# Optimization experiments

Hardware: AMD Instinct MI355X
Metric: run time of the kernel (lower is better)

Reference implementation:

```python
import jax, jax.numpy as jnp
import numpy as np


def setup_inputs() -> dict:
    key = jax.random.key(0)
    k1, k2, k3, k4, k5 = jax.random.split(key, 5)
    B, T, R, H = 64, 256, 49, 1024  # batch, caption len, regions (7x7), hidden
    V = jax.random.normal(k1, (B, R, H), dtype=jnp.float32)
    h_t = jax.random.normal(k2, (B, T, H), dtype=jnp.float32)
    Wv = jax.random.normal(k3, (R, H), dtype=jnp.float32) * (1.0 / np.sqrt(H))
    Wg = jax.random.normal(k4, (R, H), dtype=jnp.float32) * (1.0 / np.sqrt(H))
    Wh = jax.random.normal(k5, (1, R), dtype=jnp.float32) * (1.0 / np.sqrt(R))
    return {"V": V, "h_t": h_t, "Wv": Wv, "Wg": Wg, "Wh": Wh}


def reference(V, h_t, Wv, Wg, Wh):
    # content_v: [B,1,R,R] + [B,T,1,R] -> [B,T,R,R]
    cv = jnp.einsum('brh,kh->brk', V, Wv)      # [B, R, R]
    cg = jnp.einsum('bth,kh->btk', h_t, Wg)    # [B, T, R]
    content_v = cv[:, None, :, :] + cg[:, :, None, :]  # [B, T, R, R]
    # z_t = affine_h(tanh(content_v)) squeezed -> [B, T, R]
    z_t = jnp.einsum('btrk,k->btr', jnp.tanh(content_v), Wh[0])
    alpha_t = jax.nn.softmax(z_t, axis=-1)     # [B, T, R]
    c_t = jnp.einsum('btr,brh->bth', alpha_t, V)  # [B, T, H]
    return (c_t, alpha_t)
```

## Files before the change

### kernel.cpp

```cpp
#include <hip/hip_runtime.h>
#include <hip/hip_bf16.h>
#include <math.h>
#include <stdint.h>


typedef __attribute__((ext_vector_type(8))) short bf16x8;
typedef __attribute__((ext_vector_type(4))) float floatx4;

static __device__ __forceinline__ bf16x8 pack8(float4 a, float4 b) {
    union { __hip_bfloat162 h[4]; bf16x8 v; } u;
    u.h[0] = __float22bfloat162_rn(make_float2(a.x, a.y));
    u.h[1] = __float22bfloat162_rn(make_float2(a.z, a.w));
    u.h[2] = __float22bfloat162_rn(make_float2(b.x, b.y));
    u.h[3] = __float22bfloat162_rn(make_float2(b.z, b.w));
    return u.v;
}

static __device__ __forceinline__ unsigned short f2bf_bits(float f) {
    union { __hip_bfloat16 h; unsigned short u; } c;
    c.h = __float2bfloat16(f);
    return c.u;
}

__global__ __launch_bounds__(256) void gemm_mfma_tr(const float* __restrict__ Av,
                                                    const float* __restrict__ Ag,
                                                    const float* __restrict__ Wv,
                                                    const float* __restrict__ Wg,
                                                    float* __restrict__ Cv,
                                                    float* __restrict__ Cg,
                                                    unsigned short* __restrict__ vT) {
    __shared__ __align__(16) char smem[49 * 132 * 4];
    const int bid = blockIdx.x;
    const int tid = threadIdx.x;

    if (bid >= 610) {
        float* Ts = (float*)smem;
        const int tb = bid - 610;
        const int b = tb >> 3;
        const int h0 = (tb & 7) * 128;
        for (int i = tid; i < 49 * 32; i += 256) {
            const int r = i >> 5, hq = i & 31;
            *(float4*)(Ts + r * 132 + hq * 4) =
                *(const float4*)(Av + ((size_t)b * 49 + r) * 1024 + h0 + hq * 4);
        }
        __syncthreads();
        const int h = tid & 127;
        const int half = tid >> 7;
        float f[32];
#pragma unroll
        for (int j = 0; j < 32; ++j) {
            const int r = half * 32 + j;
            f[j] = (r < 49) ? Ts[r * 132 + h] : 0.f;
        }
        const size_t rowbase = ((size_t)b * 1024 + h0 + h) * 64;
#pragma unroll
        for (int o2 = 0; o2 < 4; ++o2) {
            const int o = half * 4 + o2;
            bf16x8 v = pack8(make_float4(f[o2*8+0], f[o2*8+1], f[o2*8+2], f[o2*8+3]),
                             make_float4(f[o2*8+4], f[o2*8+5], f[o2*8+6], f[o2*8+7]));
            *(bf16x8*)(vT + rowbase + (size_t)((o ^ (h & 7)) * 8)) = v;
        }
        return;
    }

    short* As = (short*)smem;
    short* Ws = (short*)(smem + 4096);
    const float* A; const float* W; float* C; int m0;
    if (bid < 98) { A = Av; W = Wv; C = Cv; m0 = bid * 32; }
    else          { A = Ag; W = Wg; C = Cg; m0 = (bid - 98) * 32; }

    const int wave = tid >> 6, lane = tid & 63;
    const int quad = lane >> 4, l16 = lane & 15;
    const int mb = (wave & 1) * 16;
    const int nb = (wave >> 1) * 32;

    floatx4 acc[2] = {};

    const int arow = tid >> 3, ag = tid & 7;
    const int wrow = tid >> 2, wq = tid & 3;
    const float* aptr = A + (size_t)(m0 + arow) * 1024 + ag * 8;
    const bool wvalid = wrow < 49;
    const float* wptr = W + (size_t)wrow * 1024 + wq * 16;

    float4 a0 = *(const float4*)(aptr);
    float4 a1 = *(const float4*)(aptr + 4);
    float4 w0 = make_float4(0.f,0.f,0.f,0.f), w1 = w0, w2 = w0, w3 = w0;
    if (wvalid) {
        w0 = *(const float4*)(wptr);
        w1 = *(const float4*)(wptr + 4);
        w2 = *(const float4*)(wptr + 8);
        w3 = *(const float4*)(wptr + 12);
    }

    for (int kc = 0; kc < 1024; kc += 64) {
        __syncthreads();
        *(bf16x8*)(As + arow * 64 + (ag ^ (arow & 7)) * 8) = pack8(a0, a1);
        *(bf16x8*)(Ws + wrow * 64 + ((wq * 2) ^ (wrow & 7)) * 8) = pack8(w0, w1);
        *(bf16x8*)(Ws + wrow * 64 + ((wq * 2 + 1) ^ (wrow & 7)) * 8) = pack8(w2, w3);
        __syncthreads();
        if (kc < 960) {
            a0 = *(const float4*)(aptr + kc + 64);
            a1 = *(const float4*)(aptr + kc + 68);
            if (wvalid) {
                w0 = *(const float4*)(wptr + kc + 64);
                w1 = *(const float4*)(wptr + kc + 68);
                w2 = *(const float4*)(wptr + kc + 72);
                w3 = *(const float4*)(wptr + kc + 76);
            }
        }
#pragma unroll
        for (int s = 0; s < 2; ++s) {
            const int am = mb + l16;
            bf16x8 af = *(const bf16x8*)(As + am * 64 + (((s << 2) + quad) ^ (am & 7)) * 8);
#pragma unroll
            for (int nt = 0; nt < 2; ++nt) {
                const int wn = nb + nt * 16 + l16;
                bf16x8 bf = *(const bf16x8*)(Ws + wn * 64 + (((s << 2) + quad) ^ (wn & 7)) * 8);
                acc[nt] = __builtin_amdgcn_mfma_f32_16x16x32_bf16(af, bf, acc[nt], 0, 0, 0);
            }
        }
    }

#pragma unroll
    for (int nt = 0; nt < 2; ++nt) {
        const int n = nb + nt * 16 + l16;
        if (n < 49) {
#pragma unroll
            for (int r = 0; r < 4; ++r) {
                const int m = m0 + mb + quad * 4 + r;
                C[(size_t)m * 49 + n] = acc[nt][r];
            }
        }
    }
}

__global__ __launch_bounds__(256) void zsoftmax(const float* __restrict__ cv,
                                                const float* __restrict__ cg,
                                                const float* __restrict__ Wh,
                                                float* __restrict__ alpha,
                                                unsigned short* __restrict__ a16) {
    const int b = blockIdx.x >> 4;
    const int t0 = (blockIdx.x & 15) * 16;
    __shared__ __align__(16) float cvl[49 * 52];
    __shared__ __align__(16) float cgl[16 * 52];
    __shared__ __align__(16) float whl[52];

    const int tid = threadIdx.x;
    for (int i = tid; i < 49 * 49; i += 256) {
        int r = i / 49, k = i - r * 49;
        cvl[r * 52 + k] = cv[(size_t)b * 2401 + i];
    }
    for (int i = tid; i < 16 * 49; i += 256) {
        int t = i / 49, k = i - t * 49;
        cgl[t * 52 + k] = cg[((size_t)b * 256 + t0) * 49 + i];
    }
    if (tid < 52) whl[tid] = (tid < 49) ? Wh[tid] : 0.f;
    __syncthreads();

    const int wave = tid >> 6;
    const int lane = tid & 63;
    const float4* cvr = (const float4*)(cvl + lane * 52);
    const float4* wh4 = (const float4*)whl;

    for (int i = 0; i < 4; ++i) {
        const int tl = wave * 4 + i;
        float z = -INFINITY;
        if (lane < 49) {
            const float4* cgr = (const float4*)(cgl + tl * 52);
            float s = 0.f;
#pragma unroll 4
            for (int kk = 0; kk < 12; ++kk) {
                float4 x = cvr[kk], g = cgr[kk], w = wh4[kk];
                float r0 = __builtin_amdgcn_rcpf(__expf(2.f * (x.x + g.x)) + 1.f);
                float r1 = __builtin_amdgcn_rcpf(__expf(2.f * (x.y + g.y)) + 1.f);
                float r2 = __builtin_amdgcn_rcpf(__expf(2.f * (x.z + g.z)) + 1.f);
                float r3 = __builtin_amdgcn_rcpf(__expf(2.f * (x.w + g.w)) + 1.f);
                s = fmaf(1.f - 2.f * r0, w.x, s);
                s = fmaf(1.f - 2.f * r1, w.y, s);
                s = fmaf(1.f - 2.f * r2, w.z, s);
                s = fmaf(1.f - 2.f * r3, w.w, s);
            }
            {
                float x = cvl[lane * 52 + 48] + cgl[tl * 52 + 48];
                float r0 = __builtin_amdgcn_rcpf(__expf(2.f * x) + 1.f);
                s = fmaf(1.f - 2.f * r0, whl[48], s);
            }
            z = s;
        }
        float m = z;
        for (int off = 32; off; off >>= 1) m = fmaxf(m, __shfl_xor(m, off));
        float p = (lane < 49) ? __expf(z - m) : 0.f;
        float sum = p;
        for (int off = 32; off; off >>= 1) sum += __shfl_xor(sum, off);
        const float val = p * __builtin_amdgcn_rcpf(sum);

        const size_t grow = (size_t)b * 256 + t0 + tl;
        if (lane < 49) alpha[grow * 49 + lane] = val;
        const int pos = (((lane >> 3) ^ (tl & 7)) << 3) | (lane & 7);
        a16[grow * 64 + pos] = f2bf_bits(val);
    }
}

__global__ __launch_bounds__(256) void ct_mfma(const unsigned short* __restrict__ a16,
                                               const unsigned short* __restrict__ vT,
                                               float* __restrict__ C) {
    const int bid = blockIdx.x;
    const int b = bid >> 5;
    const int t0 = ((bid >> 3) & 3) * 64;
    const int h0 = (bid & 7) * 128;

    __shared__ __align__(16) short Al[64 * 64];
    __shared__ __align__(16) short Vl[128 * 64];

    const int tid = threadIdx.x;
    {
        const bf16x8* src = (const bf16x8*)(a16 + ((size_t)b * 256 + t0) * 64);
        bf16x8* dst = (bf16x8*)Al;
#pragma unroll
        for (int p = 0; p < 2; ++p) dst[tid + p * 256] = src[tid + p * 256];
    }
    {
        const bf16x8* src = (const bf16x8*)(vT + ((size_t)b * 1024 + h0) * 64);
        bf16x8* dst = (bf16x8*)Vl;
#pragma unroll
        for (int p = 0; p < 4; ++p) dst[tid + p * 256] = src[tid + p * 256];
    }
    __syncthreads();

    const int wave = tid >> 6, lane = tid & 63;
    const int quad = lane >> 4, l16 = lane & 15;
    const int tb = (wave & 1) * 32;
    const int hb = (wave >> 1) * 64;

    floatx4 acc[2][4] = {};
#pragma unroll
    for (int kc = 0; kc < 2; ++kc) {
        bf16x8 af[2];
#pragma unroll
        for (int ms = 0; ms < 2; ++ms) {
            const int row = tb + ms * 16 + l16;
            af[ms] = *(const bf16x8*)(Al + row * 64 + (((kc << 2) + quad) ^ (row & 7)) * 8);
        }
#pragma unroll
        for (int ns = 0; ns < 4; ++ns) {
            const int row = hb + ns * 16 + l16;
            bf16x8 bf = *(const bf16x8*)(Vl + row * 64 + (((kc << 2) + quad) ^ (row & 7)) * 8);
#pragma unroll
            for (int ms = 0; ms < 2; ++ms)
                acc[ms][ns] = __builtin_amdgcn_mfma_f32_16x16x32_bf16(af[ms], bf, acc[ms][ns], 0, 0, 0);
        }
    }

#pragma unroll
    for (int ms = 0; ms < 2; ++ms) {
        const int t = t0 + tb + ms * 16 + quad * 4;
#pragma unroll
        for (int ns = 0; ns < 4; ++ns) {
            const int h = h0 + hb + ns * 16 + l16;
#pragma unroll
            for (int r = 0; r < 4; ++r)
                C[((size_t)b * 256 + t + r) * 1024 + h] = acc[ms][ns][r];
        }
    }
}

extern "C" void kernel_launch(void* const* d_in, const int* in_sizes, int n_in,
                              void* d_out, int out_size, void* d_ws, size_t ws_size,
                              hipStream_t stream) {
    const float* V   = (const float*)d_in[0];
    const float* h_t = (const float*)d_in[1];
    const float* Wv  = (const float*)d_in[2];
    const float* Wg  = (const float*)d_in[3];
    const float* Wh  = (const float*)d_in[4];

    float* c_t   = (float*)d_out;
    float* alpha = (float*)d_out + 16777216;

    float* cv = (float*)d_ws;
    float* cg = cv + 153664;
    unsigned short* a16 = (unsigned short*)((char*)d_ws + 3825920);
    unsigned short* vT  = a16 + 16384 * 64;

    gemm_mfma_tr<<<610 + 512, 256, 0, stream>>>(V, h_t, Wv, Wg, cv, cg, vT);
    zsoftmax<<<1024, 256, 0, stream>>>(cv, cg, Wh, alpha, a16);
    ct_mfma<<<2048, 256, 0, stream>>>(a16, vT, c_t);
}
```

Baseline: 176.8 us.

## Fuse softmax and context matmul into one kernel, keeping alpha in LDS

Merges the z/softmax kernel and the c_t MFMA kernel. Each block now handles 32 timesteps of one batch, writes the bf16 alpha tile into shared memory instead of global, then loops over 8 H-chunks of V^T, staging each chunk through LDS with a register prefetch of the next chunk. This removes the a16 global round trip and one kernel launch. In exchange the grid drops to 512 blocks, each doing more serial work with extra barriers, so parallelism is reduced while the kernel writes the large c_t output.

```diff
diff --git a/kernel.cpp b/kernel.cpp
--- a/kernel.cpp
+++ b/kernel.cpp
@@ -134,23 +134,28 @@
     }
 }
 
-__global__ __launch_bounds__(256) void zsoftmax(const float* __restrict__ cv,
-                                                const float* __restrict__ cg,
-                                                const float* __restrict__ Wh,
-                                                float* __restrict__ alpha,
-                                                unsigned short* __restrict__ a16) {
-    const int b = blockIdx.x >> 4;
-    const int t0 = (blockIdx.x & 15) * 16;
-    __shared__ __align__(16) float cvl[49 * 52];
-    __shared__ __align__(16) float cgl[16 * 52];
-    __shared__ __align__(16) float whl[52];
+__global__ __launch_bounds__(256) void zsoftmax_ct(const float* __restrict__ cv,
+                                                   const float* __restrict__ cg,
+                                                   const float* __restrict__ Wh,
+                                                   const unsigned short* __restrict__ vT,
+                                                   float* __restrict__ alpha,
+                                                   float* __restrict__ C) {
+    const int b = blockIdx.x >> 3;
+    const int t0 = (blockIdx.x & 7) * 32;
+
+    __shared__ __align__(16) char smem[4096 + 49 * 52 * 4 + 32 * 52 * 4 + 52 * 4];
+    short* Al  = (short*)smem;
+    float* cvl = (float*)(smem + 4096);
+    float* cgl = cvl + 49 * 52;
+    float* whl = cgl + 32 * 52;
+    short* Vl  = (short*)(smem + 4096);
 
     const int tid = threadIdx.x;
     for (int i = tid; i < 49 * 49; i += 256) {
         int r = i / 49, k = i - r * 49;
         cvl[r * 52 + k] = cv[(size_t)b * 2401 + i];
     }
-    for (int i = tid; i < 16 * 49; i += 256) {
+    for (int i = tid; i < 32 * 49; i += 256) {
         int t = i / 49, k = i - t * 49;
         cgl[t * 52 + k] = cg[((size_t)b * 256 + t0) * 49 + i];
     }
@@ -159,11 +164,12 @@
 
     const int wave = tid >> 6;
     const int lane = tid & 63;
+    const int quad = lane >> 4, l16 = lane & 15;
     const float4* cvr = (const float4*)(cvl + lane * 52);
     const float4* wh4 = (const float4*)whl;
 
-    for (int i = 0; i < 4; ++i) {
-        const int tl = wave * 4 + i;
+    for (int i = 0; i < 8; ++i) {
+        const int tl = wave * 8 + i;
         float z = -INFINITY;
         if (lane < 49) {
             const float4* cgr = (const float4*)(cgl + tl * 52);
@@ -197,70 +203,58 @@
         const size_t grow = (size_t)b * 256 + t0 + tl;
         if (lane < 49) alpha[grow * 49 + lane] = val;
         const int pos = (((lane >> 3) ^ (tl & 7)) << 3) | (lane & 7);
-        a16[grow * 64 + pos] = f2bf_bits(val);
-    }
-}
-
-__global__ __launch_bounds__(256) void ct_mfma(const unsigned short* __restrict__ a16,
-                                               const unsigned short* __restrict__ vT,
-                                               float* __restrict__ C) {
-    const int bid = blockIdx.x;
-    const int b = bid >> 5;
-    const int t0 = ((bid >> 3) & 3) * 64;
-    const int h0 = (bid & 7) * 128;
-
-    __shared__ __align__(16) short Al[64 * 64];
-    __shared__ __align__(16) short Vl[128 * 64];
-
-    const int tid = threadIdx.x;
+        Al[tl * 64 + pos] = (short)f2bf_bits(val);
+    }
+    __syncthreads();
+
+    const int tb = (wave & 1) * 16;
+    const int hb = (wave >> 1) * 64;
+
+    bf16x8 af[2];
     {
-        const bf16x8* src = (const bf16x8*)(a16 + ((size_t)b * 256 + t0) * 64);
-        bf16x8* dst = (bf16x8*)Al;
-#pragma unroll
-        for (int p = 0; p < 2; ++p) dst[tid + p * 256] = src[tid + p * 256];
-    }
-    {
-        const bf16x8* src = (const bf16x8*)(vT + ((size_t)b * 1024 + h0) * 64);
+        const int row = tb + l16;
+#pragma unroll
+        for (int kc = 0; kc < 2; ++kc)
+            af[kc] = *(const bf16x8*)(Al + row * 64 + (((kc << 2) + quad) ^ (row & 7)) * 8);
+    }
+
+    const bf16x8* vsrc = (const bf16x8*)(vT + ((size_t)b * 1024) * 64);
+    bf16x8 vreg[4];
+#pragma unroll
+    for (int p = 0; p < 4; ++p) vreg[p] = vsrc[tid + p * 256];
+
+    for (int c = 0; c < 8; ++c) {
         bf16x8* dst = (bf16x8*)Vl;
 #pragma unroll
-        for (int p = 0; p < 4; ++p) dst[tid + p * 256] = src[tid + p * 256];
-    }
-    __syncthreads();
-
-    const int wave = tid >> 6, lane = tid & 63;
-    const int quad = lane >> 4, l16 = lane & 15;
-    const int tb = (wave & 1) * 32;
-    const int hb = (wave >> 1) * 64;
-
-    floatx4 acc[2][4] = {};
-#pragma unroll
-    for (int kc = 0; kc < 2; ++kc) {
-        bf16x8 af[2];
-#pragma unroll
-        for (int ms = 0; ms < 2; ++ms) {
-            const int row = tb + ms * 16 + l16;
-            af[ms] = *(const bf16x8*)(Al + row * 64 + (((kc << 2) + quad) ^ (row & 7)) * 8);
-        }
-#pragma unroll
-        for (int ns = 0; ns < 4; ++ns) {
-            const int row = hb + ns * 16 + l16;
-            bf16x8 bf = *(const bf16x8*)(Vl + row * 64 + (((kc << 2) + quad) ^ (row & 7)) * 8);
-#pragma unroll
-            for (int ms = 0; ms < 2; ++ms)
-                acc[ms][ns] = __builtin_amdgcn_mfma_f32_16x16x32_bf16(af[ms], bf, acc[ms][ns], 0, 0, 0);
-        }
-    }
-
-#pragma unroll
-    for (int ms = 0; ms < 2; ++ms) {
-        const int t = t0 + tb + ms * 16 + quad * 4;
+        for (int p = 0; p < 4; ++p) dst[tid + p * 256] = vreg[p];
+        __syncthreads();
+        if (c < 7) {
+#pragma unroll
+            for (int p = 0; p < 4; ++p) vreg[p] = vsrc[(size_t)(c + 1) * 1024 + tid + p * 256];
+        }
+
+        floatx4 acc[4] = {};
+#pragma unroll
+        for (int kc = 0; kc < 2; ++kc) {
+#pragma unroll
+            for (int ns = 0; ns < 4; ++ns) {
+                const int row = hb + ns * 16 + l16;
+                bf16x8 bf = *(const bf16x8*)(Vl + row * 64 + (((kc << 2) + quad) ^ (row & 7)) * 8);
+                acc[ns] = __builtin_amdgcn_mfma_f32_16x16x32_bf16(af[kc], bf, acc[ns], 0, 0, 0);
+            }
+        }
+
+        const int h0 = c << 7;
 #pragma unroll
         for (int ns = 0; ns < 4; ++ns) {
             const int h = h0 + hb + ns * 16 + l16;
 #pragma unroll
-            for (int r = 0; r < 4; ++r)
-                C[((size_t)b * 256 + t + r) * 1024 + h] = acc[ms][ns][r];
-        }
+            for (int r = 0; r < 4; ++r) {
+                const int tg = t0 + tb + quad * 4 + r;
+                C[((size_t)b * 256 + tg) * 1024 + h] = acc[ns][r];
+            }
+        }
+        __syncthreads();
     }
 }
 
@@ -278,10 +272,8 @@
 
     float* cv = (float*)d_ws;
     float* cg = cv + 153664;
-    unsigned short* a16 = (unsigned short*)((char*)d_ws + 3825920);
-    unsigned short* vT  = a16 + 16384 * 64;
+    unsigned short* vT = (unsigned short*)((char*)d_ws + 3825920);
 
     gemm_mfma_tr<<<610 + 512, 256, 0, stream>>>(V, h_t, Wv, Wg, cv, cg, vT);
-    zsoftmax<<<1024, 256, 0, stream>>>(cv, cg, Wh, alpha, a16);
-    ct_mfma<<<2048, 256, 0, stream>>>(a16, vT, c_t);
-}
+    zsoftmax_ct<<<512, 256, 0, stream>>>(cv, cg, Wh, vT, alpha, c_t);
+}
```

Result: slower. 182.0 us (+2.9%).
